# Kernel tuning notes

Measured on AMD Instinct MI355X. Metric: run time of the kernel, lower is better.

The kernel has to match this reference:

```python
import jax, jax.numpy as jnp
import numpy as np

T, B, D, H, L = 2048, 1, 1000, 1000, 4


def _lstm_cell(x, h, c, Wih, Whh, bih, bhh):
    # x: [N, D], h/c: [N, H]; PyTorch LSTMCell gate order: i, f, g, o
    gates = x @ Wih.T + h @ Whh.T + (bih + bhh)  # [N, 4H]
    i, f, g, o = jnp.split(gates, 4, axis=-1)
    c_new = jax.nn.sigmoid(f) * c + jax.nn.sigmoid(i) * jnp.tanh(g)
    h_new = jax.nn.sigmoid(o) * jnp.tanh(c_new)
    return h_new, c_new


def setup_inputs() -> dict:
    key = jax.random.key(0)
    ks = jax.random.split(key, 5)
    s = 1.0 / np.sqrt(H)  # torch LSTMCell init scale
    return {
        "x": jax.random.normal(ks[0], (T, B, D), dtype=jnp.float32),
        "w_ih": jax.random.uniform(ks[1], (L, 4 * H, D), jnp.float32, -s, s),
        "w_hh": jax.random.uniform(ks[2], (L, 4 * H, H), jnp.float32, -s, s),
        "b_ih": jax.random.uniform(ks[3], (L, 4 * H), jnp.float32, -s, s),
        "b_hh": jax.random.uniform(ks[4], (L, 4 * H), jnp.float32, -s, s),
    }


def reference(x, w_ih, w_hh, b_ih, b_hh):
    # Hidden state is re-zeroed at every timestep in the original module, so
    # timesteps are independent: fold time*batch into one big batch [T*B, D].
    xt = x.reshape(T * B, D)
    h = jnp.zeros((T * B, H), dtype=x.dtype)
    c = jnp.zeros((T * B, H), dtype=x.dtype)
    for l in range(L):  # small fixed layer loop; each layer re-reads x[char]
        h, c = _lstm_cell(xt, h, c, w_ih[l], w_hh[l], b_ih[l], b_hh[l])
    out = h.reshape(T, B, H)  # torch.stack(ret) of [1,H] h's -> [T, 1, H]
    return jax.nn.relu(out)
```

## Files before the change

### kernel.cpp

```cpp
#include <hip/hip_runtime.h>
#include <hip/hip_bf16.h>
#include <hip/hip_fp16.h>
#include <stdint.h>


typedef unsigned short ushort_t;
typedef __bf16 bf16x8 __attribute__((ext_vector_type(8)));
typedef float f32x4 __attribute__((ext_vector_type(4)));
typedef unsigned short ushort8 __attribute__((ext_vector_type(8)));
typedef float float4v __attribute__((ext_vector_type(4)));

#define NROWS 2048
#define KPAD  2048
#define NG    4000
#define HDIM  1000
#define BM 128
#define BN 128
#define BK 32

#define GLOBAL_AS __attribute__((address_space(1)))
#define LDS_AS    __attribute__((address_space(3)))

__device__ __forceinline__ ushort_t f2bf(float f) {
  union { float f; uint32_t u; } x; x.f = f;
  uint32_t u = x.u;
  return (ushort_t)((u + 0x7FFFu + ((u >> 16) & 1u)) >> 16);
}

__device__ __forceinline__ float sigf(float v)   { return 1.f / (1.f + __expf(-v)); }
__device__ __forceinline__ float tanhft(float v) { return 2.f / (1.f + __expf(-2.f * v)) - 1.f; }

__global__ __launch_bounds__(256) void convert_w_kernel(
    const float* __restrict__ wih, const float* __restrict__ whh,
    ushort_t* __restrict__ W) {
  const int l = blockIdx.z;
  const int j = blockIdx.y;
  const int k0 = threadIdx.x * 8;
  const size_t rowIdx = (size_t)l * NG + j;
  ushort8 out = {0,0,0,0,0,0,0,0};
  const float* src = nullptr;
  if (k0 < 1000)                        src = wih + rowIdx * 1000 + k0;
  else if (k0 >= 1024 && k0 < 2024)     src = whh + rowIdx * 1000 + (k0 - 1024);
  if (src) {
    float4v v0 = *(const float4v*)(src);
    float4v v1 = *(const float4v*)(src + 4);
    out[0]=f2bf(v0[0]); out[1]=f2bf(v0[1]); out[2]=f2bf(v0[2]); out[3]=f2bf(v0[3]);
    out[4]=f2bf(v1[0]); out[5]=f2bf(v1[1]); out[6]=f2bf(v1[2]); out[7]=f2bf(v1[3]);
  }
  *(ushort8*)&W[(rowIdx << 11) + k0] = out;
}

__global__ __launch_bounds__(256) void convert_x_kernel(
    const float* __restrict__ x, ushort_t* __restrict__ A) {
  const int n = blockIdx.y;
  const int k0 = threadIdx.x * 8;
  ushort8 out = {0,0,0,0,0,0,0,0};
  if (k0 < 1000) {
    const float* src = x + (size_t)n * 1000 + k0;
    float4v v0 = *(const float4v*)(src);
    float4v v1 = *(const float4v*)(src + 4);
    out[0]=f2bf(v0[0]); out[1]=f2bf(v0[1]); out[2]=f2bf(v0[2]); out[3]=f2bf(v0[3]);
    out[4]=f2bf(v1[0]); out[5]=f2bf(v1[1]); out[6]=f2bf(v1[2]); out[7]=f2bf(v1[3]);
  }
  *(ushort8*)&A[((size_t)n << 11) + k0] = out;
}

__global__ __launch_bounds__(256, 2) void gemm_kernel(
    const ushort_t* __restrict__ Abuf,
    const ushort_t* __restrict__ Wbuf,
    __half* __restrict__ gates,
    int kend) {
  __shared__ __align__(16) ushort_t As[3][BM * BK];
  __shared__ __align__(16) ushort_t Bs[3][BN * BK];
  const int tid  = threadIdx.x;
  const int wave = tid >> 6;
  const int lane = tid & 63;
  const int rowBase = blockIdx.y * BM;
  const int colBase = blockIdx.x * BN;
  const int wr = wave >> 1, wc = wave & 1;
  const int rl = lane & 15, kq = lane >> 4;
  const int NT = kend >> 5;

  f32x4 acc[4][4] = {};

  auto stage = [&](int buf, int k0) {
    #pragma unroll
    for (int r = 0; r < 2; ++r) {
      const int be  = (r * 4 + wave) * 512;
      const int e   = be + lane * 8;
      const int row = e >> 5;
      const int kk  = e & 31;
      const ushort_t* g = Abuf + (size_t)(rowBase + row) * KPAD + k0 + kk;
      __builtin_amdgcn_global_load_lds((GLOBAL_AS void*)g,
                                       (LDS_AS void*)&As[buf][be], 16, 0, 0);
    }
    #pragma unroll
    for (int r = 0; r < 2; ++r) {
      const int be  = (r * 4 + wave) * 512;
      const int e   = be + lane * 8;
      int row = colBase + (e >> 5);
      if (row > NG - 1) row = NG - 1;
      const int kk  = e & 31;
      const ushort_t* g = Wbuf + (size_t)row * KPAD + k0 + kk;
      __builtin_amdgcn_global_load_lds((GLOBAL_AS void*)g,
                                       (LDS_AS void*)&Bs[buf][be], 16, 0, 0);
    }
  };

  stage(0, 0);
  stage(1, BK);

  int cur = 0;
  for (int t = 0; t < NT; ++t) {
    if (t + 2 < NT) {
      int nb = cur + 2; if (nb >= 3) nb -= 3;
      stage(nb, (t + 2) * BK);
      asm volatile("s_waitcnt vmcnt(8)" ::: "memory");
    } else if (t + 2 == NT) {
      asm volatile("s_waitcnt vmcnt(4)" ::: "memory");
    } else {
      asm volatile("s_waitcnt vmcnt(0)" ::: "memory");
    }
    __builtin_amdgcn_s_barrier();
    __builtin_amdgcn_sched_barrier(0);

    bf16x8 af[4], bfr[4];
    #pragma unroll
    for (int i = 0; i < 4; ++i)
      af[i] = *(const bf16x8*)&As[cur][(wr * 64 + i * 16 + rl) * BK + kq * 8];
    #pragma unroll
    for (int i = 0; i < 4; ++i)
      bfr[i] = *(const bf16x8*)&Bs[cur][(wc * 64 + i * 16 + rl) * BK + kq * 8];

    asm volatile("s_waitcnt lgkmcnt(0)" ::: "memory");
    __builtin_amdgcn_sched_barrier(0);
    __builtin_amdgcn_s_barrier();

    __builtin_amdgcn_s_setprio(1);
    #pragma unroll
    for (int mi = 0; mi < 4; ++mi)
      #pragma unroll
      for (int ni = 0; ni < 4; ++ni)
        acc[mi][ni] = __builtin_amdgcn_mfma_f32_16x16x32_bf16(
            af[mi], bfr[ni], acc[mi][ni], 0, 0, 0);
    __builtin_amdgcn_s_setprio(0);

    cur = cur + 1; if (cur >= 3) cur = 0;
  }

  #pragma unroll
  for (int mi = 0; mi < 4; ++mi) {
    #pragma unroll
    for (int ni = 0; ni < 4; ++ni) {
      const int col = colBase + wc * 64 + ni * 16 + rl;
      if (col < NG) {
        const int row0 = rowBase + wr * 64 + mi * 16 + kq * 4;
        #pragma unroll
        for (int q = 0; q < 4; ++q)
          gates[(size_t)(row0 + q) * NG + col] = __float2half(acc[mi][ni][q]);
      }
    }
  }
}

__global__ __launch_bounds__(256) void lstm_ew_kernel(
    const __half* __restrict__ gates,
    const float* __restrict__ bih,
    const float* __restrict__ bhh,
    float* __restrict__ c,
    ushort_t* __restrict__ A,
    float* __restrict__ out,
    int layer) {
  const int j = blockIdx.x * 256 + threadIdx.x;
  if (j >= HDIM) return;
  const int n = blockIdx.y;
  const size_t gbase = (size_t)n * NG;
  const float ig = __half2float(gates[gbase + j])        + bih[j]        + bhh[j];
  const float fg = __half2float(gates[gbase + 1000 + j]) + bih[1000 + j] + bhh[1000 + j];
  const float gg = __half2float(gates[gbase + 2000 + j]) + bih[2000 + j] + bhh[2000 + j];
  const float og = __half2float(gates[gbase + 3000 + j]) + bih[3000 + j] + bhh[3000 + j];
  const float cp = (layer == 0) ? 0.f : c[(size_t)n * HDIM + j];
  const float cn = sigf(fg) * cp + sigf(ig) * tanhft(gg);
  const float hn = sigf(og) * tanhft(cn);
  c[(size_t)n * HDIM + j] = cn;
  A[((size_t)n << 11) + 1024 + j] = f2bf(hn);
  if (layer == 3) out[(size_t)n * HDIM + j] = fmaxf(hn, 0.f);
}

extern "C" void kernel_launch(void* const* d_in, const int* in_sizes, int n_in,
                              void* d_out, int out_size, void* d_ws, size_t ws_size,
                              hipStream_t stream) {
  const float* x   = (const float*)d_in[0];
  const float* wih = (const float*)d_in[1];
  const float* whh = (const float*)d_in[2];
  const float* bih = (const float*)d_in[3];
  const float* bhh = (const float*)d_in[4];
  float* out = (float*)d_out;

  char* ws = (char*)d_ws;
  ushort_t* A     = (ushort_t*)ws;
  ushort_t* W     = (ushort_t*)(ws + 8388608ull);
  __half*   gates = (__half*)(ws + 73924608ull);
  float*    c     = (float*)(ws + 90308608ull);

  convert_w_kernel<<<dim3(1, 4000, 4), 256, 0, stream>>>(wih, whh, W);
  convert_x_kernel<<<dim3(1, 2048, 1), 256, 0, stream>>>(x, A);

  for (int l = 0; l < 4; ++l) {
    const int kend = (l == 0) ? 1024 : 2048;
    gemm_kernel<<<dim3(32, 16), 256, 0, stream>>>(
        A, W + (size_t)l * NG * KPAD, gates, kend);
    lstm_ew_kernel<<<dim3(4, 2048), 256, 0, stream>>>(
        gates, bih + l * NG, bhh + l * NG, c, A, out, l);
  }
}
```

Before: 238.4 us.

## Fuse LSTM elementwise into GEMM epilogue with gate-interleaved weights and swizzled LDS

Weight rows are reordered so the four gates for each hidden unit are interleaved, padded to 4096 columns. This lets each GEMM tile hold complete i/f/g/o groups and apply the LSTM cell update in its epilogue through an LDS staging buffer. That removes the fp16 gates round trip to global memory and the separate elementwise launch per layer. It also adds an XOR swizzle on LDS tiles to reduce bank conflicts, double-buffers the hidden state, and precomputes summed biases. The cost is extra syncs and a serial two-pass epilogue inside the GEMM.

New measurement: 206.3 us. 1.16x faster.

```diff
diff --git a/kernel.cpp b/kernel.cpp
--- a/kernel.cpp
+++ b/kernel.cpp
@@ -1,6 +1,5 @@
 #include <hip/hip_runtime.h>
 #include <hip/hip_bf16.h>
-#include <hip/hip_fp16.h>
 #include <stdint.h>
 
 
@@ -10,9 +9,9 @@
 typedef unsigned short ushort8 __attribute__((ext_vector_type(8)));
 typedef float float4v __attribute__((ext_vector_type(4)));
 
-#define NROWS 2048
+#define XK    1024
 #define KPAD  2048
-#define NG    4000
+#define NG2   4096
 #define HDIM  1000
 #define BM 128
 #define BN 128
@@ -34,26 +33,29 @@
     const float* __restrict__ wih, const float* __restrict__ whh,
     ushort_t* __restrict__ W) {
   const int l = blockIdx.z;
-  const int j = blockIdx.y;
+  const int c = blockIdx.y;
+  const int j = c >> 2, g = c & 3;
   const int k0 = threadIdx.x * 8;
-  const size_t rowIdx = (size_t)l * NG + j;
   ushort8 out = {0,0,0,0,0,0,0,0};
-  const float* src = nullptr;
-  if (k0 < 1000)                        src = wih + rowIdx * 1000 + k0;
-  else if (k0 >= 1024 && k0 < 2024)     src = whh + rowIdx * 1000 + (k0 - 1024);
-  if (src) {
-    float4v v0 = *(const float4v*)(src);
-    float4v v1 = *(const float4v*)(src + 4);
-    out[0]=f2bf(v0[0]); out[1]=f2bf(v0[1]); out[2]=f2bf(v0[2]); out[3]=f2bf(v0[3]);
-    out[4]=f2bf(v1[0]); out[5]=f2bf(v1[1]); out[6]=f2bf(v1[2]); out[7]=f2bf(v1[3]);
-  }
-  *(ushort8*)&W[(rowIdx << 11) + k0] = out;
+  if (j < HDIM) {
+    const size_t srow = (size_t)l * 4000 + g * 1000 + j;
+    const float* src = nullptr;
+    if (k0 < 1000)                        src = wih + srow * 1000 + k0;
+    else if (k0 >= 1024 && k0 < 2024)     src = whh + srow * 1000 + (k0 - 1024);
+    if (src) {
+      float4v v0 = *(const float4v*)(src);
+      float4v v1 = *(const float4v*)(src + 4);
+      out[0]=f2bf(v0[0]); out[1]=f2bf(v0[1]); out[2]=f2bf(v0[2]); out[3]=f2bf(v0[3]);
+      out[4]=f2bf(v1[0]); out[5]=f2bf(v1[1]); out[6]=f2bf(v1[2]); out[7]=f2bf(v1[3]);
+    }
+  }
+  *(ushort8*)&W[((size_t)l * NG2 + c) * KPAD + k0] = out;
 }
 
 __global__ __launch_bounds__(256) void convert_x_kernel(
-    const float* __restrict__ x, ushort_t* __restrict__ A) {
-  const int n = blockIdx.y;
-  const int k0 = threadIdx.x * 8;
+    const float* __restrict__ x, ushort_t* __restrict__ Xb) {
+  const int n  = blockIdx.y * 2 + (threadIdx.x >> 7);
+  const int k0 = (threadIdx.x & 127) * 8;
   ushort8 out = {0,0,0,0,0,0,0,0};
   if (k0 < 1000) {
     const float* src = x + (size_t)n * 1000 + k0;
@@ -62,16 +64,37 @@
     out[0]=f2bf(v0[0]); out[1]=f2bf(v0[1]); out[2]=f2bf(v0[2]); out[3]=f2bf(v0[3]);
     out[4]=f2bf(v1[0]); out[5]=f2bf(v1[1]); out[6]=f2bf(v1[2]); out[7]=f2bf(v1[3]);
   }
-  *(ushort8*)&A[((size_t)n << 11) + k0] = out;
+  *(ushort8*)&Xb[((size_t)n << 10) + k0] = out;
+}
+
+__global__ __launch_bounds__(256) void bias_kernel(
+    const float* __restrict__ bih, const float* __restrict__ bhh,
+    float* __restrict__ bsum) {
+  const int l = blockIdx.y;
+  const int c = blockIdx.x * 256 + threadIdx.x;
+  const int j = c >> 2, g = c & 3;
+  float v = 0.f;
+  if (j < HDIM) {
+    const int r = l * 4000 + g * 1000 + j;
+    v = bih[r] + bhh[r];
+  }
+  bsum[(size_t)l * NG2 + c] = v;
 }
 
 __global__ __launch_bounds__(256, 2) void gemm_kernel(
-    const ushort_t* __restrict__ Abuf,
-    const ushort_t* __restrict__ Wbuf,
-    __half* __restrict__ gates,
-    int kend) {
-  __shared__ __align__(16) ushort_t As[3][BM * BK];
-  __shared__ __align__(16) ushort_t Bs[3][BN * BK];
+    const ushort_t* __restrict__ Xb,
+    const ushort_t* __restrict__ Hin,
+    const ushort_t* __restrict__ Wl,
+    const float* __restrict__ bsum,
+    float* __restrict__ cbuf,
+    ushort_t* __restrict__ Hout,
+    float* __restrict__ out,
+    int layer, int kend) {
+  __shared__ __align__(16) char smem[49152];
+  ushort_t (*As)[BM * BK] = (ushort_t (*)[BM * BK])smem;
+  ushort_t (*Bs)[BN * BK] = (ushort_t (*)[BN * BK])(smem + 24576);
+  float* ex = (float*)smem;
+
   const int tid  = threadIdx.x;
   const int wave = tid >> 6;
   const int lane = tid & 63;
@@ -84,24 +107,22 @@
   f32x4 acc[4][4] = {};
 
   auto stage = [&](int buf, int k0) {
+    const ushort_t* asrc = (k0 < XK) ? (Xb + k0) : (Hin + (k0 - XK));
     #pragma unroll
     for (int r = 0; r < 2; ++r) {
       const int be  = (r * 4 + wave) * 512;
-      const int e   = be + lane * 8;
-      const int row = e >> 5;
-      const int kk  = e & 31;
-      const ushort_t* g = Abuf + (size_t)(rowBase + row) * KPAD + k0 + kk;
+      const int row = (be >> 5) + (lane >> 2);
+      const int sl  = (lane & 3) ^ ((row >> 1) & 3);
+      const ushort_t* g = asrc + (size_t)(rowBase + row) * XK + sl * 8;
       __builtin_amdgcn_global_load_lds((GLOBAL_AS void*)g,
                                        (LDS_AS void*)&As[buf][be], 16, 0, 0);
     }
     #pragma unroll
     for (int r = 0; r < 2; ++r) {
       const int be  = (r * 4 + wave) * 512;
-      const int e   = be + lane * 8;
-      int row = colBase + (e >> 5);
-      if (row > NG - 1) row = NG - 1;
-      const int kk  = e & 31;
-      const ushort_t* g = Wbuf + (size_t)row * KPAD + k0 + kk;
+      const int row = (be >> 5) + (lane >> 2);
+      const int sl  = (lane & 3) ^ ((row >> 1) & 3);
+      const ushort_t* g = Wl + (size_t)(colBase + row) * KPAD + k0 + sl * 8;
       __builtin_amdgcn_global_load_lds((GLOBAL_AS void*)g,
                                        (LDS_AS void*)&Bs[buf][be], 16, 0, 0);
     }
@@ -126,11 +147,15 @@
 
     bf16x8 af[4], bfr[4];
     #pragma unroll
-    for (int i = 0; i < 4; ++i)
-      af[i] = *(const bf16x8*)&As[cur][(wr * 64 + i * 16 + rl) * BK + kq * 8];
-    #pragma unroll
-    for (int i = 0; i < 4; ++i)
-      bfr[i] = *(const bf16x8*)&Bs[cur][(wc * 64 + i * 16 + rl) * BK + kq * 8];
+    for (int i = 0; i < 4; ++i) {
+      const int ar = wr * 64 + i * 16 + rl;
+      af[i] = *(const bf16x8*)&As[cur][ar * BK + ((kq ^ ((ar >> 1) & 3)) * 8)];
+    }
+    #pragma unroll
+    for (int i = 0; i < 4; ++i) {
+      const int br = wc * 64 + i * 16 + rl;
+      bfr[i] = *(const bf16x8*)&Bs[cur][br * BK + ((kq ^ ((br >> 1) & 3)) * 8)];
+    }
 
     asm volatile("s_waitcnt lgkmcnt(0)" ::: "memory");
     __builtin_amdgcn_sched_barrier(0);
@@ -148,43 +173,47 @@
     cur = cur + 1; if (cur >= 3) cur = 0;
   }
 
+  const int jTile = blockIdx.x * 32;
   #pragma unroll
-  for (int mi = 0; mi < 4; ++mi) {
-    #pragma unroll
-    for (int ni = 0; ni < 4; ++ni) {
-      const int col = colBase + wc * 64 + ni * 16 + rl;
-      if (col < NG) {
-        const int row0 = rowBase + wr * 64 + mi * 16 + kq * 4;
+  for (int h = 0; h < 2; ++h) {
+    __syncthreads();
+    if (wr == h) {
+      #pragma unroll
+      for (int mi = 0; mi < 4; ++mi) {
+        const int lr = mi * 16 + kq * 4;
         #pragma unroll
-        for (int q = 0; q < 4; ++q)
-          gates[(size_t)(row0 + q) * NG + col] = __float2half(acc[mi][ni][q]);
+        for (int ni = 0; ni < 4; ++ni) {
+          const int lc = wc * 64 + ni * 16 + rl;
+          #pragma unroll
+          for (int q = 0; q < 4; ++q)
+            ex[(lr + q) * 132 + lc] = acc[mi][ni][q];
+        }
       }
     }
-  }
-}
-
-__global__ __launch_bounds__(256) void lstm_ew_kernel(
-    const __half* __restrict__ gates,
-    const float* __restrict__ bih,
-    const float* __restrict__ bhh,
-    float* __restrict__ c,
-    ushort_t* __restrict__ A,
-    float* __restrict__ out,
-    int layer) {
-  const int j = blockIdx.x * 256 + threadIdx.x;
-  if (j >= HDIM) return;
-  const int n = blockIdx.y;
-  const size_t gbase = (size_t)n * NG;
-  const float ig = __half2float(gates[gbase + j])        + bih[j]        + bhh[j];
-  const float fg = __half2float(gates[gbase + 1000 + j]) + bih[1000 + j] + bhh[1000 + j];
-  const float gg = __half2float(gates[gbase + 2000 + j]) + bih[2000 + j] + bhh[2000 + j];
-  const float og = __half2float(gates[gbase + 3000 + j]) + bih[3000 + j] + bhh[3000 + j];
-  const float cp = (layer == 0) ? 0.f : c[(size_t)n * HDIM + j];
-  const float cn = sigf(fg) * cp + sigf(ig) * tanhft(gg);
-  const float hn = sigf(og) * tanhft(cn);
-  c[(size_t)n * HDIM + j] = cn;
-  A[((size_t)n << 11) + 1024 + j] = f2bf(hn);
-  if (layer == 3) out[(size_t)n * HDIM + j] = fmaxf(hn, 0.f);
+    __syncthreads();
+    #pragma unroll
+    for (int p = 0; p < 8; ++p) {
+      const int idx = p * 256 + tid;
+      const int lr  = idx >> 5;
+      const int j   = idx & 31;
+      const int jg  = jTile + j;
+      if (jg < HDIM) {
+        const int n = rowBase + h * 64 + lr;
+        float4v gv = *(const float4v*)&ex[lr * 132 + 4 * j];
+        float4v bv = *(const float4v*)&bsum[(size_t)(jTile + j) * 4];
+        const float ig = gv[0] + bv[0];
+        const float fg = gv[1] + bv[1];
+        const float gg = gv[2] + bv[2];
+        const float og = gv[3] + bv[3];
+        const float cp = (layer == 0) ? 0.f : cbuf[(size_t)n * HDIM + jg];
+        const float cn = sigf(fg) * cp + sigf(ig) * tanhft(gg);
+        const float hn = sigf(og) * tanhft(cn);
+        cbuf[(size_t)n * HDIM + jg] = cn;
+        Hout[((size_t)n << 10) + jg] = f2bf(hn);
+        if (layer == 3) out[(size_t)n * HDIM + jg] = fmaxf(hn, 0.f);
+      }
+    }
+  }
 }
 
 extern "C" void kernel_launch(void* const* d_in, const int* in_sizes, int n_in,
@@ -198,19 +227,23 @@
   float* out = (float*)d_out;
 
   char* ws = (char*)d_ws;
-  ushort_t* A     = (ushort_t*)ws;
-  ushort_t* W     = (ushort_t*)(ws + 8388608ull);
-  __half*   gates = (__half*)(ws + 73924608ull);
-  float*    c     = (float*)(ws + 90308608ull);
-
-  convert_w_kernel<<<dim3(1, 4000, 4), 256, 0, stream>>>(wih, whh, W);
-  convert_x_kernel<<<dim3(1, 2048, 1), 256, 0, stream>>>(x, A);
+  ushort_t* Xb   = (ushort_t*)ws;
+  ushort_t* Hb   = (ushort_t*)(ws + 4194304ull);
+  ushort_t* W    = (ushort_t*)(ws + 12582912ull);
+  float*    bsum = (float*)(ws + 79691776ull);
+  float*    cbuf = (float*)(ws + 79757312ull);
+  const size_t NH = 2048ull * 1024ull;
+
+  convert_w_kernel<<<dim3(1, 4096, 4), 256, 0, stream>>>(wih, whh, W);
+  convert_x_kernel<<<dim3(1, 1024), 256, 0, stream>>>(x, Xb);
+  bias_kernel<<<dim3(16, 4), 256, 0, stream>>>(bih, bhh, bsum);
 
   for (int l = 0; l < 4; ++l) {
     const int kend = (l == 0) ? 1024 : 2048;
+    const ushort_t* Hin  = Hb + (size_t)(l & 1) * NH;
+    ushort_t*       Hout = Hb + (size_t)((l + 1) & 1) * NH;
     gemm_kernel<<<dim3(32, 16), 256, 0, stream>>>(
-        A, W + (size_t)l * NG * KPAD, gates, kend);
-    lstm_ew_kernel<<<dim3(4, 2048), 256, 0, stream>>>(
-        gates, bih + l * NG, bhh + l * NG, c, A, out, l);
-  }
-}
+        Xb, Hin, W + (size_t)l * NG2 * KPAD, bsum + (size_t)l * NG2,
+        cbuf, Hout, out, l, kend);
+  }
+}
```
